# Optimization experiments

Measured on AMD Instinct MI355X. Metric: run time of the kernel, lower is better.

Reference implementation:

```python
import jax, jax.numpy as jnp
import numpy as np

DIM = 1024
N_HEADS = 16
HEAD_DIM = DIM // N_HEADS
SCALE = HEAD_DIM ** (-0.5)


def setup_inputs() -> dict:
    key = jax.random.key(0)
    ks = jax.random.split(key, 5)
    B, N = 2, 2048
    x = jax.random.normal(ks[0], (B, N, DIM), dtype=jnp.float32)
    # torch nn.Linear weight layout: (out_features, in_features)
    qkv_w = jax.random.normal(ks[1], (3 * DIM, DIM), dtype=jnp.float32) * 0.02
    qkv_b = jax.random.normal(ks[2], (3 * DIM,), dtype=jnp.float32) * 0.02
    proj_w = jax.random.normal(ks[3], (DIM, DIM), dtype=jnp.float32) * 0.02
    proj_b = jax.random.normal(ks[4], (DIM,), dtype=jnp.float32) * 0.02
    return {"x": x, "qkv_w": qkv_w, "qkv_b": qkv_b, "proj_w": proj_w, "proj_b": proj_b}


def reference(x, qkv_w, qkv_b, proj_w, proj_b):
    B, N, C = x.shape
    # QKV projection: (B,N,C) -> (B,N,3C)
    qkv = jnp.einsum('bnc,oc->bno', x, qkv_w) + qkv_b
    # (B,N,3,H,Dh) -> (3,B,H,N,Dh)
    qkv = qkv.reshape(B, N, 3, N_HEADS, HEAD_DIM).transpose(2, 0, 3, 1, 4)
    q, k, v = qkv[0], qkv[1], qkv[2]
    attn = jnp.einsum('bhqd,bhkd->bhqk', q, k) * SCALE
    attn = jax.nn.softmax(attn, axis=-1)
    out = jnp.einsum('bhqk,bhkd->bhqd', attn, v)
    out = out.transpose(0, 2, 1, 3).reshape(B, N, C)  # concat heads
    out = jnp.einsum('bnc,oc->bno', out, proj_w) + proj_b
    return out
```

## Files before the change

kernel.cpp:

```cpp
#include <hip/hip_runtime.h>

#define DIM 1024
#define NHEADS 16
#define HD 64
#define NSEQ 2048
#define MROWS 4096
#define QKV_LD 3072

typedef __attribute__((ext_vector_type(8))) short short8;
typedef __attribute__((ext_vector_type(4))) short short4v;
typedef __attribute__((ext_vector_type(4))) float f32x4;

typedef __attribute__((address_space(1))) void gvoid_t;
typedef __attribute__((address_space(3))) void lvoid_t;

#if __has_builtin(__builtin_amdgcn_exp2f)
#define EXP2(x) __builtin_amdgcn_exp2f(x)
#else
#define EXP2(x) exp2f(x)
#endif

#if __has_builtin(__builtin_amdgcn_mfma_f32_16x16x16_bf16)
#define MFMA16(a, b, c) __builtin_amdgcn_mfma_f32_16x16x16_bf16(a, b, c, 0, 0, 0)
#elif __has_builtin(__builtin_amdgcn_mfma_f32_16x16x16bf16_1k)
#define MFMA16(a, b, c) __builtin_amdgcn_mfma_f32_16x16x16bf16_1k(a, b, c, 0, 0, 0)
#else
static __device__ __forceinline__ f32x4 mfma16_asm(short4v a, short4v b, f32x4 c) {
  __asm__("v_mfma_f32_16x16x16_bf16 %0, %1, %2, %0" : "+v"(c) : "v"(a), "v"(b));
  return c;
}
#define MFMA16(a, b, c) mfma16_asm(a, b, c)
#endif

#define EXP_SCALE 0.18033688011112042f

__device__ __forceinline__ unsigned short f2bf(float f) {
  unsigned int u = __builtin_bit_cast(unsigned int, f);
  u += 0x7FFFu + ((u >> 16) & 1u);
  return (unsigned short)(u >> 16);
}

__device__ __forceinline__ void gl_lds16(const void* g, void* l) {
  __builtin_amdgcn_global_load_lds((gvoid_t*)g, (lvoid_t*)l, 16, 0, 0);
}

__global__ __launch_bounds__(256) void cast_bf16_3(
    const float* __restrict__ x, const float* __restrict__ wq,
    const float* __restrict__ wp,
    unsigned short* __restrict__ xb, unsigned short* __restrict__ wqb,
    unsigned short* __restrict__ wpb)
{
  int g = blockIdx.x * 256 + threadIdx.x;
  const float* src;
  unsigned short* dst;
  if (g < 1048576)            { src = x  + (size_t)g * 4;              dst = xb  + (size_t)g * 4; }
  else if (g < 1048576 + 786432) { int t = g - 1048576; src = wq + (size_t)t * 4; dst = wqb + (size_t)t * 4; }
  else                        { int t = g - 1048576 - 786432; src = wp + (size_t)t * 4; dst = wpb + (size_t)t * 4; }
  float4 v = *(const float4*)src;
  ushort4 o;
  o.x = f2bf(v.x); o.y = f2bf(v.y); o.z = f2bf(v.z); o.w = f2bf(v.w);
  *(ushort4*)dst = o;
}

__global__ __launch_bounds__(256) void gemm_nt(
    const unsigned short* __restrict__ A,
    const unsigned short* __restrict__ Bw,
    const float* __restrict__ bias,
    int K, int mode,
    unsigned short* __restrict__ oq,
    unsigned short* __restrict__ ovt,
    float* __restrict__ of)
{
  __shared__ unsigned short As[128 * 32];
  __shared__ unsigned short Bs[128 * 32];

  const int tid  = threadIdx.x;
  const int wave = tid >> 6, lane = tid & 63;
  const int quad = lane >> 4, l15 = lane & 15;
  const int mblk = blockIdx.x * 128;
  const int nblk = blockIdx.y * 128;
  const int wrow = (wave >> 1) * 64, wcol = (wave & 1) * 64;

  f32x4 acc[4][4] = {};

  const int sr = lane >> 2;
  const int sq = (lane & 3) ^ (sr & 3);
  const unsigned short* aBase = A  + (size_t)(mblk + wave * 32 + sr) * K + sq * 8;
  const unsigned short* bBase = Bw + (size_t)(nblk + wave * 32 + sr) * K + sq * 8;

  for (int k0 = 0; k0 < K; k0 += 32) {
    __syncthreads();
    gl_lds16(aBase + k0,          As + (wave * 32) * 32);
    gl_lds16(aBase + 16 * K + k0, As + (wave * 32 + 16) * 32);
    gl_lds16(bBase + k0,          Bs + (wave * 32) * 32);
    gl_lds16(bBase + 16 * K + k0, Bs + (wave * 32 + 16) * 32);
    __syncthreads();

    short8 af[4], bf8[4];
#pragma unroll
    for (int mt = 0; mt < 4; ++mt) {
      int row = wrow + mt * 16 + l15;
      af[mt] = *(const short8*)(As + row * 32 + ((quad ^ (row & 3)) * 8));
    }
#pragma unroll
    for (int nt = 0; nt < 4; ++nt) {
      int row = wcol + nt * 16 + l15;
      bf8[nt] = *(const short8*)(Bs + row * 32 + ((quad ^ (row & 3)) * 8));
    }
#pragma unroll
    for (int mt = 0; mt < 4; ++mt)
#pragma unroll
      for (int nt = 0; nt < 4; ++nt)
        acc[mt][nt] = __builtin_amdgcn_mfma_f32_16x16x32_bf16(af[mt], bf8[nt], acc[mt][nt], 0, 0, 0);
  }

  float bv[4];
#pragma unroll
  for (int nt = 0; nt < 4; ++nt) bv[nt] = bias[nblk + wcol + nt * 16 + l15];

  if (mode == 0) {
#pragma unroll
    for (int mt = 0; mt < 4; ++mt) {
      int row0 = mblk + wrow + mt * 16 + quad * 4;
#pragma unroll
      for (int nt = 0; nt < 4; ++nt) {
        int col = nblk + wcol + nt * 16 + l15;
#pragma unroll
        for (int r = 0; r < 4; ++r)
          of[(size_t)(row0 + r) * DIM + col] = acc[mt][nt][r] + bv[nt];
      }
    }
  } else if (nblk < 2048) {
#pragma unroll
    for (int mt = 0; mt < 4; ++mt) {
      int row0 = mblk + wrow + mt * 16 + quad * 4;
#pragma unroll
      for (int nt = 0; nt < 4; ++nt) {
        int col = nblk + wcol + nt * 16 + l15;
#pragma unroll
        for (int r = 0; r < 4; ++r)
          oq[(size_t)(row0 + r) * QKV_LD + col] = f2bf(acc[mt][nt][r] + bv[nt]);
      }
    }
  } else {
#pragma unroll
    for (int mt = 0; mt < 4; ++mt) {
      int row0 = mblk + wrow + mt * 16 + quad * 4;
      int n0 = row0 & (NSEQ - 1);
      int bb = row0 >> 11;
#pragma unroll
      for (int nt = 0; nt < 4; ++nt) {
        int colr = (nblk - 2048) + wcol + nt * 16 + l15;
        int bh = bb * NHEADS + (colr >> 6);
        int d  = colr & 63;
        ushort4 pk;
        pk.x = f2bf(acc[mt][nt][0] + bv[nt]);
        pk.y = f2bf(acc[mt][nt][1] + bv[nt]);
        pk.z = f2bf(acc[mt][nt][2] + bv[nt]);
        pk.w = f2bf(acc[mt][nt][3] + bv[nt]);
        *(ushort4*)(ovt + ((size_t)bh * HD + d) * NSEQ + n0) = pk;
      }
    }
  }
}

__global__ __launch_bounds__(256) void gemm_nt64(
    const unsigned short* __restrict__ A,
    const unsigned short* __restrict__ Bw,
    const float* __restrict__ bias,
    int K,
    float* __restrict__ of)
{
  __shared__ unsigned short As[64 * 32];
  __shared__ unsigned short Bs[128 * 32];

  const int tid  = threadIdx.x;
  const int wave = tid >> 6, lane = tid & 63;
  const int quad = lane >> 4, l15 = lane & 15;
  const int mblk = blockIdx.x * 64;
  const int nblk = blockIdx.y * 128;
  const int wrow = (wave >> 1) * 32, wcol = (wave & 1) * 64;

  f32x4 acc[2][4] = {};

  const int sr = lane >> 2;
  const int sq = (lane & 3) ^ (sr & 3);
  const unsigned short* aBase = A  + (size_t)(mblk + wave * 16 + sr) * K + sq * 8;
  const unsigned short* bBase = Bw + (size_t)(nblk + wave * 32 + sr) * K + sq * 8;

  for (int k0 = 0; k0 < K; k0 += 32) {
    __syncthreads();
    gl_lds16(aBase + k0,          As + (wave * 16) * 32);
    gl_lds16(bBase + k0,          Bs + (wave * 32) * 32);
    gl_lds16(bBase + 16 * K + k0, Bs + (wave * 32 + 16) * 32);
    __syncthreads();

    short8 af[2], bf8[4];
#pragma unroll
    for (int mt = 0; mt < 2; ++mt) {
      int row = wrow + mt * 16 + l15;
      af[mt] = *(const short8*)(As + row * 32 + ((quad ^ (row & 3)) * 8));
    }
#pragma unroll
    for (int nt = 0; nt < 4; ++nt) {
      int row = wcol + nt * 16 + l15;
      bf8[nt] = *(const short8*)(Bs + row * 32 + ((quad ^ (row & 3)) * 8));
    }
#pragma unroll
    for (int mt = 0; mt < 2; ++mt)
#pragma unroll
      for (int nt = 0; nt < 4; ++nt)
        acc[mt][nt] = __builtin_amdgcn_mfma_f32_16x16x32_bf16(af[mt], bf8[nt], acc[mt][nt], 0, 0, 0);
  }

  float bv[4];
#pragma unroll
  for (int nt = 0; nt < 4; ++nt) bv[nt] = bias[nblk + wcol + nt * 16 + l15];

#pragma unroll
  for (int mt = 0; mt < 2; ++mt) {
    int row0 = mblk + wrow + mt * 16 + quad * 4;
#pragma unroll
    for (int nt = 0; nt < 4; ++nt) {
      int col = nblk + wcol + nt * 16 + l15;
#pragma unroll
      for (int r = 0; r < 4; ++r)
        of[(size_t)(row0 + r) * DIM + col] = acc[mt][nt][r] + bv[nt];
    }
  }
}

__global__ __launch_bounds__(256, 4) void attn_fused(
    const unsigned short* __restrict__ qkv,
    const unsigned short* __restrict__ vt,
    unsigned short* __restrict__ aout)
{
  __shared__ unsigned short Ks[64 * 64];
  __shared__ unsigned short Vs[64 * 64];

  const int tid  = threadIdx.x;
  const int wave = tid >> 6, lane = tid & 63;
  const int quad = lane >> 4, l15 = lane & 15;
  const int bh = blockIdx.x, b = bh >> 4, h = bh & 15;
  const int q0 = blockIdx.y * 64;
  const size_t qkvB = (size_t)b * NSEQ * QKV_LD;

  short8 qf[2];
#pragma unroll
  for (int ks = 0; ks < 2; ++ks)
    qf[ks] = *(const short8*)(qkv + qkvB +
        (size_t)(q0 + wave * 16 + l15) * QKV_LD + h * HD + ks * 32 + quad * 8);

  f32x4 oacc[4] = {};
  float lsum = 0.f;

  const int sr8 = lane >> 3;
  const int sp8 = lane & 7;

  const unsigned short* kBase = qkv + qkvB + DIM + h * HD;
  const unsigned short* vBase = vt + (size_t)bh * HD * NSEQ;

  for (int kk = 0; kk < NSEQ; kk += 64) {
    __syncthreads();
#pragma unroll
    for (int i = 0; i < 2; ++i) {
      int r  = wave * 16 + i * 8 + sr8;
      int qc = sp8 ^ (r & 7);
      gl_lds16(kBase + (size_t)(kk + r) * QKV_LD + qc * 8, Ks + (wave * 16 + i * 8) * 64);
      gl_lds16(vBase + (size_t)r * NSEQ + kk + qc * 8,     Vs + (wave * 16 + i * 8) * 64);
    }
    __syncthreads();

    short8 kf[4][2];
#pragma unroll
    for (int kt = 0; kt < 4; ++kt)
#pragma unroll
      for (int ks = 0; ks < 2; ++ks) {
        int row = kt * 16 + l15;
        kf[kt][ks] = *(const short8*)(Ks + row * 64 + (((ks * 4 + quad) ^ (row & 7)) * 8));
      }

    f32x4 sacc[4] = {};
#pragma unroll
    for (int kt = 0; kt < 4; ++kt) {
      sacc[kt] = __builtin_amdgcn_mfma_f32_16x16x32_bf16(kf[kt][0], qf[0], sacc[kt], 0, 0, 0);
      sacc[kt] = __builtin_amdgcn_mfma_f32_16x16x32_bf16(kf[kt][1], qf[1], sacc[kt], 0, 0, 0);
    }

    short4v vf[4][4];
#pragma unroll
    for (int dt = 0; dt < 4; ++dt) {
      int row = dt * 16 + l15;
      int rw  = row & 7;
      const unsigned short* vb = Vs + row * 64 + (quad & 1) * 4;
#pragma unroll
      for (int kt = 0; kt < 4; ++kt) {
        int phys = (2 * kt + (quad >> 1)) ^ rw;
        vf[dt][kt] = *(const short4v*)(vb + phys * 8);
      }
    }

#pragma unroll
    for (int kt = 0; kt < 4; ++kt) {
      float p0 = EXP2(sacc[kt][0] * EXP_SCALE);
      float p1 = EXP2(sacc[kt][1] * EXP_SCALE);
      float p2 = EXP2(sacc[kt][2] * EXP_SCALE);
      float p3 = EXP2(sacc[kt][3] * EXP_SCALE);
      lsum += (p0 + p1) + (p2 + p3);
      unsigned r0 = __builtin_bit_cast(unsigned, p0) + 0x8000u;
      unsigned r1 = __builtin_bit_cast(unsigned, p1) + 0x8000u;
      unsigned r2 = __builtin_bit_cast(unsigned, p2) + 0x8000u;
      unsigned r3 = __builtin_bit_cast(unsigned, p3) + 0x8000u;
      uint2 pd;
      pd.x = __builtin_amdgcn_perm(r1, r0, 0x07060302u);
      pd.y = __builtin_amdgcn_perm(r3, r2, 0x07060302u);
      short4v pf = __builtin_bit_cast(short4v, pd);
#pragma unroll
      for (int dt = 0; dt < 4; ++dt)
        oacc[dt] = MFMA16(vf[dt][kt], pf, oacc[dt]);
    }
  }

  lsum += __shfl_xor(lsum, 16);
  lsum += __shfl_xor(lsum, 32);
  float inv = 1.0f / lsum;

  const int qrow = q0 + wave * 16 + l15;
  const size_t outBase = (size_t)(b * NSEQ + qrow) * DIM + h * HD;
#pragma unroll
  for (int dt = 0; dt < 4; ++dt) {
    unsigned a0 = __builtin_bit_cast(unsigned, oacc[dt][0] * inv) + 0x8000u;
    unsigned a1 = __builtin_bit_cast(unsigned, oacc[dt][1] * inv) + 0x8000u;
    unsigned a2 = __builtin_bit_cast(unsigned, oacc[dt][2] * inv) + 0x8000u;
    unsigned a3 = __builtin_bit_cast(unsigned, oacc[dt][3] * inv) + 0x8000u;
    uint2 st;
    st.x = __builtin_amdgcn_perm(a1, a0, 0x07060302u);
    st.y = __builtin_amdgcn_perm(a3, a2, 0x07060302u);
    *(uint2*)(aout + outBase + dt * 16 + quad * 4) = st;
  }
}

extern "C" void kernel_launch(void* const* d_in, const int* in_sizes, int n_in,
                              void* d_out, int out_size, void* d_ws, size_t ws_size,
                              hipStream_t stream) {
  (void)in_sizes; (void)n_in; (void)out_size; (void)ws_size;
  const float* x      = (const float*)d_in[0];
  const float* qkv_w  = (const float*)d_in[1];
  const float* qkv_b  = (const float*)d_in[2];
  const float* proj_w = (const float*)d_in[3];
  const float* proj_b = (const float*)d_in[4];
  float* out = (float*)d_out;

  char* ws = (char*)d_ws;
  unsigned short* xb   = (unsigned short*)(ws);
  unsigned short* wqb  = (unsigned short*)(ws + ( 8u << 20));
  unsigned short* wpb  = (unsigned short*)(ws + (14u << 20));
  unsigned short* qkv  = (unsigned short*)(ws + (16u << 20));
  unsigned short* vtw  = (unsigned short*)(ws + (40u << 20));
  unsigned short* attn = (unsigned short*)(ws + (48u << 20));

  cast_bf16_3<<<8192, 256, 0, stream>>>(x, qkv_w, proj_w, xb, wqb, wpb);
  gemm_nt<<<dim3(32, 24), 256, 0, stream>>>(xb, wqb, qkv_b, DIM, 1, qkv, vtw, nullptr);
  attn_fused<<<dim3(32, 32), 256, 0, stream>>>(qkv, vtw, attn);
  gemm_nt64<<<dim3(64, 8), 256, 0, stream>>>(attn, wpb, proj_b, DIM, out);
}
```

Baseline: 197.8 us.

## Split KV across waves with double-buffered per-wave staging and LDS reduction

Restructures attention so each wave processes all 64 query rows over a disjoint KV subset, loading K/V tiles into per-wave double-buffered LDS slabs without block-wide barriers. V^T is stored in a tiled 16-column layout to make the loads contiguous. The partial outputs and row sums are then combined across waves through LDS float atomics. This removes the per-iteration __syncthreads and overlaps loads with compute. In exchange it raises register and LDS use (occupancy hint drops from 4 to 3) and adds an atomic reduction epilogue.

```diff
diff --git a/kernel.cpp b/kernel.cpp
--- a/kernel.cpp
+++ b/kernel.cpp
@@ -31,6 +31,8 @@
 }
 #define MFMA16(a, b, c) mfma16_asm(a, b, c)
 #endif
+
+#define MFMA32(a, b, c) __builtin_amdgcn_mfma_f32_16x16x32_bf16(a, b, c, 0, 0, 0)
 
 #define EXP_SCALE 0.18033688011112042f
 
@@ -111,7 +113,7 @@
     for (int mt = 0; mt < 4; ++mt)
 #pragma unroll
       for (int nt = 0; nt < 4; ++nt)
-        acc[mt][nt] = __builtin_amdgcn_mfma_f32_16x16x32_bf16(af[mt], bf8[nt], acc[mt][nt], 0, 0, 0);
+        acc[mt][nt] = MFMA32(af[mt], bf8[nt], acc[mt][nt]);
   }
 
   float bv[4];
@@ -158,7 +160,7 @@
         pk.y = f2bf(acc[mt][nt][1] + bv[nt]);
         pk.z = f2bf(acc[mt][nt][2] + bv[nt]);
         pk.w = f2bf(acc[mt][nt][3] + bv[nt]);
-        *(ushort4*)(ovt + ((size_t)bh * HD + d) * NSEQ + n0) = pk;
+        *(ushort4*)(ovt + (size_t)bh * 131072 + (n0 >> 4) * 1024 + d * 16 + (n0 & 15)) = pk;
       }
     }
   }
@@ -210,7 +212,7 @@
     for (int mt = 0; mt < 2; ++mt)
 #pragma unroll
       for (int nt = 0; nt < 4; ++nt)
-        acc[mt][nt] = __builtin_amdgcn_mfma_f32_16x16x32_bf16(af[mt], bf8[nt], acc[mt][nt], 0, 0, 0);
+        acc[mt][nt] = MFMA32(af[mt], bf8[nt], acc[mt][nt]);
   }
 
   float bv[4];
@@ -230,13 +232,14 @@
   }
 }
 
-__global__ __launch_bounds__(256, 4) void attn_fused(
+__global__ __launch_bounds__(256, 3) void attn_fused(
     const unsigned short* __restrict__ qkv,
-    const unsigned short* __restrict__ vt,
+    const unsigned short* __restrict__ vt2,
     unsigned short* __restrict__ aout)
 {
-  __shared__ unsigned short Ks[64 * 64];
-  __shared__ unsigned short Vs[64 * 64];
+  __shared__ unsigned short stage[2][4][2048];
+  __shared__ float accS[4096];
+  __shared__ float lsumS[64];
 
   const int tid  = threadIdx.x;
   const int wave = tid >> 6, lane = tid & 63;
@@ -245,68 +248,49 @@
   const int q0 = blockIdx.y * 64;
   const size_t qkvB = (size_t)b * NSEQ * QKV_LD;
 
-  short8 qf[2];
-#pragma unroll
-  for (int ks = 0; ks < 2; ++ks)
-    qf[ks] = *(const short8*)(qkv + qkvB +
-        (size_t)(q0 + wave * 16 + l15) * QKV_LD + h * HD + ks * 32 + quad * 8);
-
-  f32x4 oacc[4] = {};
-  float lsum = 0.f;
-
-  const int sr8 = lane >> 3;
-  const int sp8 = lane & 7;
-
-  const unsigned short* kBase = qkv + qkvB + DIM + h * HD;
-  const unsigned short* vBase = vt + (size_t)bh * HD * NSEQ;
-
-  for (int kk = 0; kk < NSEQ; kk += 64) {
-    __syncthreads();
-#pragma unroll
-    for (int i = 0; i < 2; ++i) {
-      int r  = wave * 16 + i * 8 + sr8;
-      int qc = sp8 ^ (r & 7);
-      gl_lds16(kBase + (size_t)(kk + r) * QKV_LD + qc * 8, Ks + (wave * 16 + i * 8) * 64);
-      gl_lds16(vBase + (size_t)r * NSEQ + kk + qc * 8,     Vs + (wave * 16 + i * 8) * 64);
-    }
-    __syncthreads();
-
-    short8 kf[4][2];
-#pragma unroll
-    for (int kt = 0; kt < 4; ++kt)
-#pragma unroll
-      for (int ks = 0; ks < 2; ++ks) {
-        int row = kt * 16 + l15;
-        kf[kt][ks] = *(const short8*)(Ks + row * 64 + (((ks * 4 + quad) ^ (row & 7)) * 8));
-      }
-
+  for (int i = tid; i < 4096; i += 256) accS[i] = 0.f;
+  if (tid < 64) lsumS[tid] = 0.f;
+  __syncthreads();
+
+  short8 qf[4][2];
+#pragma unroll
+  for (int qt = 0; qt < 4; ++qt)
+#pragma unroll
+    for (int ks = 0; ks < 2; ++ks)
+      qf[qt][ks] = *(const short8*)(qkv + qkvB +
+          (size_t)(q0 + qt * 16 + l15) * QKV_LD + h * HD + ks * 32 + quad * 8);
+
+  const int sr8 = lane >> 3, sp8 = lane & 7;
+  const unsigned short* kStage = qkv + qkvB + DIM + h * HD
+      + (size_t)(wave * 16 + sr8) * QKV_LD + (sp8 ^ sr8) * 8;
+  const unsigned short* vStage = vt2 + (size_t)bh * 131072 + wave * 1024 + lane * 8;
+
+  unsigned short* slab0 = &stage[0][wave][0];
+  unsigned short* slab1 = &stage[1][wave][0];
+
+  f32x4 oacc[4][4] = {};
+  float lsum[4] = {};
+
+  auto compute = [&](const unsigned short* cur) {
+    short8 kf0 = *(const short8*)(cur + l15 * 64 + ((quad       ^ (l15 & 7)) * 8));
+    short8 kf1 = *(const short8*)(cur + l15 * 64 + (((4 + quad) ^ (l15 & 7)) * 8));
     f32x4 sacc[4] = {};
 #pragma unroll
-    for (int kt = 0; kt < 4; ++kt) {
-      sacc[kt] = __builtin_amdgcn_mfma_f32_16x16x32_bf16(kf[kt][0], qf[0], sacc[kt], 0, 0, 0);
-      sacc[kt] = __builtin_amdgcn_mfma_f32_16x16x32_bf16(kf[kt][1], qf[1], sacc[kt], 0, 0, 0);
-    }
-
-    short4v vf[4][4];
-#pragma unroll
-    for (int dt = 0; dt < 4; ++dt) {
-      int row = dt * 16 + l15;
-      int rw  = row & 7;
-      const unsigned short* vb = Vs + row * 64 + (quad & 1) * 4;
-#pragma unroll
-      for (int kt = 0; kt < 4; ++kt) {
-        int phys = (2 * kt + (quad >> 1)) ^ rw;
-        vf[dt][kt] = *(const short4v*)(vb + phys * 8);
-      }
-    }
-
-#pragma unroll
-    for (int kt = 0; kt < 4; ++kt) {
-      float p0 = EXP2(sacc[kt][0] * EXP_SCALE);
-      float p1 = EXP2(sacc[kt][1] * EXP_SCALE);
-      float p2 = EXP2(sacc[kt][2] * EXP_SCALE);
-      float p3 = EXP2(sacc[kt][3] * EXP_SCALE);
-      lsum += (p0 + p1) + (p2 + p3);
+    for (int qt = 0; qt < 4; ++qt) {
+      sacc[qt] = MFMA32(kf0, qf[qt][0], sacc[qt]);
+      sacc[qt] = MFMA32(kf1, qf[qt][1], sacc[qt]);
+    }
+    short4v vf[4];
+#pragma unroll
+    for (int dt = 0; dt < 4; ++dt)
+      vf[dt] = *(const short4v*)(cur + 1024 + (dt * 16 + l15) * 16 + quad * 4);
+#pragma unroll
+    for (int qt = 0; qt < 4; ++qt) {
+      float p0 = EXP2(sacc[qt][0] * EXP_SCALE);
+      float p1 = EXP2(sacc[qt][1] * EXP_SCALE);
+      float p2 = EXP2(sacc[qt][2] * EXP_SCALE);
+      float p3 = EXP2(sacc[qt][3] * EXP_SCALE);
+      lsum[qt] += (p0 + p1) + (p2 + p3);
       unsigned r0 = __builtin_bit_cast(unsigned, p0) + 0x8000u;
       unsigned r1 = __builtin_bit_cast(unsigned, p1) + 0x8000u;
       unsigned r2 = __builtin_bit_cast(unsigned, p2) + 0x8000u;
@@ -317,26 +301,59 @@
       short4v pf = __builtin_bit_cast(short4v, pd);
 #pragma unroll
       for (int dt = 0; dt < 4; ++dt)
-        oacc[dt] = MFMA16(vf[dt][kt], pf, oacc[dt]);
-    }
-  }
-
-  lsum += __shfl_xor(lsum, 16);
-  lsum += __shfl_xor(lsum, 32);
-  float inv = 1.0f / lsum;
-
-  const int qrow = q0 + wave * 16 + l15;
-  const size_t outBase = (size_t)(b * NSEQ + qrow) * DIM + h * HD;
-#pragma unroll
-  for (int dt = 0; dt < 4; ++dt) {
-    unsigned a0 = __builtin_bit_cast(unsigned, oacc[dt][0] * inv) + 0x8000u;
-    unsigned a1 = __builtin_bit_cast(unsigned, oacc[dt][1] * inv) + 0x8000u;
-    unsigned a2 = __builtin_bit_cast(unsigned, oacc[dt][2] * inv) + 0x8000u;
-    unsigned a3 = __builtin_bit_cast(unsigned, oacc[dt][3] * inv) + 0x8000u;
-    uint2 st;
-    st.x = __builtin_amdgcn_perm(a1, a0, 0x07060302u);
-    st.y = __builtin_amdgcn_perm(a3, a2, 0x07060302u);
-    *(uint2*)(aout + outBase + dt * 16 + quad * 4) = st;
+        oacc[dt][qt] = MFMA16(vf[dt], pf, oacc[dt][qt]);
+    }
+  };
+
+  gl_lds16(kStage,                 slab0);
+  gl_lds16(kStage + 8 * QKV_LD,    slab0 + 512);
+  gl_lds16(vStage,                 slab0 + 1024);
+  gl_lds16(vStage + 512,           slab0 + 1536);
+
+  const unsigned short* kNext = kStage + (size_t)64 * QKV_LD;
+  const unsigned short* vNext = vStage + 4096;
+
+#pragma unroll 2
+  for (int t = 0; t < 31; ++t) {
+    unsigned short* cur = (t & 1) ? slab1 : slab0;
+    unsigned short* nxt = (t & 1) ? slab0 : slab1;
+    gl_lds16(kNext,                nxt);
+    gl_lds16(kNext + 8 * QKV_LD,   nxt + 512);
+    gl_lds16(vNext,                nxt + 1024);
+    gl_lds16(vNext + 512,          nxt + 1536);
+    kNext += (size_t)64 * QKV_LD;
+    vNext += 4096;
+    __asm__ volatile("s_waitcnt vmcnt(4)" ::: "memory");
+    compute(cur);
+  }
+  __asm__ volatile("s_waitcnt vmcnt(0)" ::: "memory");
+  compute(slab1);
+
+#pragma unroll
+  for (int qt = 0; qt < 4; ++qt) {
+    float s = lsum[qt];
+    s += __shfl_xor(s, 16);
+    s += __shfl_xor(s, 32);
+    if (quad == 0) atomicAdd(&lsumS[qt * 16 + l15], s);
+  }
+#pragma unroll
+  for (int dt = 0; dt < 4; ++dt)
+#pragma unroll
+    for (int qt = 0; qt < 4; ++qt) {
+      int q = qt * 16 + l15;
+      int dbase = dt * 16 + quad * 4;
+#pragma unroll
+      for (int r = 0; r < 4; ++r)
+        atomicAdd(&accS[q * 64 + ((dbase + r + q) & 63)], oacc[dt][qt][r]);
+    }
+  __syncthreads();
+
+  const int d = lane;
+  for (int qq = 0; qq < 16; ++qq) {
+    int q = wave * 16 + qq;
+    float inv = 1.0f / lsumS[q];
+    float v = accS[q * 64 + ((d + q) & 63)] * inv;
+    aout[(size_t)(b * NSEQ + q0 + q) * DIM + h * HD + d] = f2bf(v);
   }
 }
 
```

Result: slower. 482.0 us (+143.6%).

## Pre-tile V into fragment layout, load V directly to registers, fold softmax scale into Q

Applied to the files above, without the earlier changes.

The QKV GEMM epilogue now writes V in a tiled layout matching the MFMA fragment order, so the attention kernel loads V fragments straight from global memory into registers instead of staging them through LDS. The Q columns are pre-multiplied by the exp2 softmax scale in the GEMM epilogue, which removes a multiply per score in the attention inner loop. Launch bounds drop from 4 to 2 blocks per SM, allowing more registers for the direct V loads. The risks are global-load latency on V without LDS reuse, lower occupancy, and bf16 rounding of the pre-scaled Q.

```diff
diff --git a/kernel.cpp b/kernel.cpp
--- a/kernel.cpp
+++ b/kernel.cpp
@@ -31,6 +31,8 @@
 }
 #define MFMA16(a, b, c) mfma16_asm(a, b, c)
 #endif
+
+#define MFMA32(a, b, c) __builtin_amdgcn_mfma_f32_16x16x32_bf16(a, b, c, 0, 0, 0)
 
 #define EXP_SCALE 0.18033688011112042f
 
@@ -111,7 +113,7 @@
     for (int mt = 0; mt < 4; ++mt)
 #pragma unroll
       for (int nt = 0; nt < 4; ++nt)
-        acc[mt][nt] = __builtin_amdgcn_mfma_f32_16x16x32_bf16(af[mt], bf8[nt], acc[mt][nt], 0, 0, 0);
+        acc[mt][nt] = MFMA32(af[mt], bf8[nt], acc[mt][nt]);
   }
 
   float bv[4];
@@ -131,6 +133,7 @@
       }
     }
   } else if (nblk < 2048) {
+    const float qs = (nblk < 1024) ? EXP_SCALE : 1.0f;
 #pragma unroll
     for (int mt = 0; mt < 4; ++mt) {
       int row0 = mblk + wrow + mt * 16 + quad * 4;
@@ -139,7 +142,7 @@
         int col = nblk + wcol + nt * 16 + l15;
 #pragma unroll
         for (int r = 0; r < 4; ++r)
-          oq[(size_t)(row0 + r) * QKV_LD + col] = f2bf(acc[mt][nt][r] + bv[nt]);
+          oq[(size_t)(row0 + r) * QKV_LD + col] = f2bf((acc[mt][nt][r] + bv[nt]) * qs);
       }
     }
   } else {
@@ -158,7 +161,7 @@
         pk.y = f2bf(acc[mt][nt][1] + bv[nt]);
         pk.z = f2bf(acc[mt][nt][2] + bv[nt]);
         pk.w = f2bf(acc[mt][nt][3] + bv[nt]);
-        *(ushort4*)(ovt + ((size_t)bh * HD + d) * NSEQ + n0) = pk;
+        *(ushort4*)(ovt + (size_t)bh * 131072 + (n0 >> 4) * 1024 + d * 16 + (n0 & 15)) = pk;
       }
     }
   }
@@ -210,7 +213,7 @@
     for (int mt = 0; mt < 2; ++mt)
 #pragma unroll
       for (int nt = 0; nt < 4; ++nt)
-        acc[mt][nt] = __builtin_amdgcn_mfma_f32_16x16x32_bf16(af[mt], bf8[nt], acc[mt][nt], 0, 0, 0);
+        acc[mt][nt] = MFMA32(af[mt], bf8[nt], acc[mt][nt]);
   }
 
   float bv[4];
@@ -230,13 +233,12 @@
   }
 }
 
-__global__ __launch_bounds__(256, 4) void attn_fused(
+__global__ __launch_bounds__(256, 2) void attn_fused(
     const unsigned short* __restrict__ qkv,
-    const unsigned short* __restrict__ vt,
+    const unsigned short* __restrict__ vt2,
     unsigned short* __restrict__ aout)
 {
   __shared__ unsigned short Ks[64 * 64];
-  __shared__ unsigned short Vs[64 * 64];
 
   const int tid  = threadIdx.x;
   const int wave = tid >> 6, lane = tid & 63;
@@ -256,56 +258,48 @@
 
   const int sr8 = lane >> 3;
   const int sp8 = lane & 7;
+  const int sqc = sp8 ^ sr8;
 
   const unsigned short* kBase = qkv + qkvB + DIM + h * HD;
-  const unsigned short* vBase = vt + (size_t)bh * HD * NSEQ;
-
-  for (int kk = 0; kk < NSEQ; kk += 64) {
+  const unsigned short* vBase = vt2 + (size_t)bh * 131072 + l15 * 16 + quad * 4;
+
+  for (int t = 0; t < 32; ++t) {
     __syncthreads();
 #pragma unroll
     for (int i = 0; i < 2; ++i) {
-      int r  = wave * 16 + i * 8 + sr8;
-      int qc = sp8 ^ (r & 7);
-      gl_lds16(kBase + (size_t)(kk + r) * QKV_LD + qc * 8, Ks + (wave * 16 + i * 8) * 64);
-      gl_lds16(vBase + (size_t)r * NSEQ + kk + qc * 8,     Vs + (wave * 16 + i * 8) * 64);
-    }
+      int r = t * 64 + wave * 16 + i * 8 + sr8;
+      gl_lds16(kBase + (size_t)r * QKV_LD + sqc * 8, Ks + (wave * 16 + i * 8) * 64);
+    }
+    short4v vf[4][4];
+#pragma unroll
+    for (int dt = 0; dt < 4; ++dt)
+#pragma unroll
+      for (int g = 0; g < 4; ++g)
+        vf[dt][g] = *(const short4v*)(vBase + t * 4096 + g * 1024 + dt * 256);
     __syncthreads();
 
     short8 kf[4][2];
 #pragma unroll
-    for (int kt = 0; kt < 4; ++kt)
+    for (int g = 0; g < 4; ++g)
 #pragma unroll
       for (int ks = 0; ks < 2; ++ks) {
-        int row = kt * 16 + l15;
-        kf[kt][ks] = *(const short8*)(Ks + row * 64 + (((ks * 4 + quad) ^ (row & 7)) * 8));
+        int row = g * 16 + l15;
+        kf[g][ks] = *(const short8*)(Ks + row * 64 + (((ks * 4 + quad) ^ (row & 7)) * 8));
       }
 
     f32x4 sacc[4] = {};
 #pragma unroll
-    for (int kt = 0; kt < 4; ++kt) {
-      sacc[kt] = __builtin_amdgcn_mfma_f32_16x16x32_bf16(kf[kt][0], qf[0], sacc[kt], 0, 0, 0);
-      sacc[kt] = __builtin_amdgcn_mfma_f32_16x16x32_bf16(kf[kt][1], qf[1], sacc[kt], 0, 0, 0);
-    }
-
-    short4v vf[4][4];
-#pragma unroll
-    for (int dt = 0; dt < 4; ++dt) {
-      int row = dt * 16 + l15;
-      int rw  = row & 7;
-      const unsigned short* vb = Vs + row * 64 + (quad & 1) * 4;
-#pragma unroll
-      for (int kt = 0; kt < 4; ++kt) {
-        int phys = (2 * kt + (quad >> 1)) ^ rw;
-        vf[dt][kt] = *(const short4v*)(vb + phys * 8);
-      }
-    }
-
-#pragma unroll
-    for (int kt = 0; kt < 4; ++kt) {
-      float p0 = EXP2(sacc[kt][0] * EXP_SCALE);
-      float p1 = EXP2(sacc[kt][1] * EXP_SCALE);
-      float p2 = EXP2(sacc[kt][2] * EXP_SCALE);
-      float p3 = EXP2(sacc[kt][3] * EXP_SCALE);
+    for (int g = 0; g < 4; ++g) {
+      sacc[g] = MFMA32(kf[g][0], qf[0], sacc[g]);
+      sacc[g] = MFMA32(kf[g][1], qf[1], sacc[g]);
+    }
+
+#pragma unroll
+    for (int g = 0; g < 4; ++g) {
+      float p0 = EXP2(sacc[g][0]);
+      float p1 = EXP2(sacc[g][1]);
+      float p2 = EXP2(sacc[g][2]);
+      float p3 = EXP2(sacc[g][3]);
       lsum += (p0 + p1) + (p2 + p3);
       unsigned r0 = __builtin_bit_cast(unsigned, p0) + 0x8000u;
       unsigned r1 = __builtin_bit_cast(unsigned, p1) + 0x8000u;
@@ -317,7 +311,7 @@
       short4v pf = __builtin_bit_cast(short4v, pd);
 #pragma unroll
       for (int dt = 0; dt < 4; ++dt)
-        oacc[dt] = MFMA16(vf[dt][kt], pf, oacc[dt]);
+        oacc[dt] = MFMA16(vf[dt][g], pf, oacc[dt]);
     }
   }
 
```

Measured after the change: 214.8 us. 8.6% more time.
